# Optimization experiments

Measured on AMD Instinct MI355X. Metric: run time of the kernel, lower is better.

## Reference

```python
import jax, jax.numpy as jnp
import numpy as np

EMBED_DIM = 1024
NUM_HEADS = 16
HEAD_DIM = EMBED_DIM // NUM_HEADS
B, QL, CL = 2, 2048, 2048


def setup_inputs() -> dict:
    key = jax.random.key(0)
    ks = jax.random.split(key, 10)
    s = 1.0 / np.sqrt(EMBED_DIM)  # torch Linear default init scale (approx)
    inp = {
        "query": jax.random.normal(ks[0], (B, QL, EMBED_DIM), jnp.float32),
        "context": jax.random.normal(ks[1], (B, CL, EMBED_DIM), jnp.float32),
        "Wq": jax.random.normal(ks[2], (EMBED_DIM, EMBED_DIM), jnp.float32) * s,
        "bq": jnp.zeros((EMBED_DIM,), jnp.float32),
        "Wk": jax.random.normal(ks[3], (EMBED_DIM, EMBED_DIM), jnp.float32) * s,
        "bk": jnp.zeros((EMBED_DIM,), jnp.float32),
        "Wv": jax.random.normal(ks[4], (EMBED_DIM, EMBED_DIM), jnp.float32) * s,
        "bv": jnp.zeros((EMBED_DIM,), jnp.float32),
        "Wo": jax.random.normal(ks[5], (EMBED_DIM, EMBED_DIM), jnp.float32) * s,
        "bo": jnp.zeros((EMBED_DIM,), jnp.float32),
    }
    return inp


def reference(query, context, Wq, bq, Wk, bk, Wv, bv, Wo, bo):
    b, ql, _ = query.shape
    cl = context.shape[1]
    # projections (torch Linear: x @ W.T + b; here W stored as (in, out) so x @ W + b)
    Q = (query @ Wq + bq).reshape(b, ql, NUM_HEADS, HEAD_DIM).transpose(0, 2, 1, 3)
    K = (context @ Wk + bk).reshape(b, cl, NUM_HEADS, HEAD_DIM).transpose(0, 2, 1, 3)
    V = (context @ Wv + bv).reshape(b, cl, NUM_HEADS, HEAD_DIM).transpose(0, 2, 1, 3)
    # scores [b, h, ql, cl]
    scores = jnp.einsum("bhqd,bhkd->bhqk", Q, K) / np.sqrt(HEAD_DIM).astype(np.float32)
    probs = jax.nn.softmax(scores, axis=-1)
    # dropout=0.0 (eval): identity
    attended = jnp.einsum("bhqk,bhkd->bhqd", probs, V)
    attended = attended.transpose(0, 2, 1, 3).reshape(b, ql, EMBED_DIM)
    return attended @ Wo + bo
```

## Files before the change

### kernel.cpp

```cpp
#include <hip/hip_runtime.h>
#include <hip/hip_bf16.h>
#include <stdint.h>

#define EMBED 1024
#define NH 16
#define HD 64
#define BATCH 2
#define QLEN 2048
#define CLEN 2048

typedef short short8 __attribute__((ext_vector_type(8)));
typedef unsigned short ushort8v __attribute__((ext_vector_type(8)));
typedef float f32x4 __attribute__((ext_vector_type(4)));

__device__ __forceinline__ void async_load16(const void* g, void* l) {
    __builtin_amdgcn_global_load_lds((const __attribute__((address_space(1))) void*)g,
                                     (__attribute__((address_space(3))) void*)l, 16, 0, 0);
}

__global__ void cvt_two(const float* __restrict__ a, __hip_bfloat16* __restrict__ oa,
                        const float* __restrict__ b2, __hip_bfloat16* __restrict__ ob) {
    const float* src = blockIdx.y ? b2 : a;
    __hip_bfloat16* dst = blockIdx.y ? ob : oa;
    int i = (blockIdx.x * 256 + threadIdx.x) * 4;
    float4 v = *(const float4*)(src + i);
    __hip_bfloat16 h[4];
    h[0] = __float2bfloat16(v.x);
    h[1] = __float2bfloat16(v.y);
    h[2] = __float2bfloat16(v.z);
    h[3] = __float2bfloat16(v.w);
    *(ushort4*)(dst + i) = *(const ushort4*)h;
}

__global__ void wtrans4(const float* __restrict__ W0, const float* __restrict__ W1,
                        const float* __restrict__ W2, const float* __restrict__ W3,
                        __hip_bfloat16* __restrict__ T0, __hip_bfloat16* __restrict__ T1,
                        __hip_bfloat16* __restrict__ T2, __hip_bfloat16* __restrict__ T3) {
    const int z = blockIdx.z;
    const float* W = z == 0 ? W0 : z == 1 ? W1 : z == 2 ? W2 : W3;
    __hip_bfloat16* Wt = z == 0 ? T0 : z == 1 ? T1 : z == 2 ? T2 : T3;
    __shared__ float t[32][33];
    const int tx = threadIdx.x, ty = threadIdx.y;
    const int n0 = blockIdx.x * 32, k0 = blockIdx.y * 32;
#pragma unroll
    for (int r = 0; r < 4; r++)
        t[ty * 4 + r][tx] = W[(size_t)(k0 + ty * 4 + r) * EMBED + n0 + tx];
    __syncthreads();
#pragma unroll
    for (int r = 0; r < 4; r++)
        Wt[(size_t)(n0 + ty * 4 + r) * EMBED + k0 + tx] = __float2bfloat16(t[tx][ty * 4 + r]);
}

__global__ __launch_bounds__(256) void vtrans(const __hip_bfloat16* __restrict__ V,
                                              __hip_bfloat16* __restrict__ Vt) {
    __shared__ unsigned short t[64][65];
    const int tid = threadIdx.x;
    const int c0 = blockIdx.x * 64;
    const int b = blockIdx.y >> 4, h = blockIdx.y & 15;
    const int r = tid >> 2;
    const int cs = (tid & 3) * 16;
    const unsigned short* src = (const unsigned short*)V + (size_t)(b * CLEN + c0 + r) * EMBED + h * HD + cs;
    ushort8v v0 = *(const ushort8v*)src;
    ushort8v v1 = *(const ushort8v*)(src + 8);
#pragma unroll
    for (int j = 0; j < 8; j++) { t[r][cs + j] = v0[j]; t[r][cs + 8 + j] = v1[j]; }
    __syncthreads();
    const int d = tid >> 2;
    const int ts = (tid & 3) * 16;
    ushort8v o0, o1;
#pragma unroll
    for (int j = 0; j < 8; j++) { o0[j] = t[ts + j][d]; o1[j] = t[ts + 8 + j][d]; }
    unsigned short* dst = (unsigned short*)Vt + (size_t)((b * NH + h) * HD + d) * CLEN + c0 + ts;
    *(ushort8v*)dst = o0;
    *(ushort8v*)(dst + 8) = o1;
}

__device__ __forceinline__ void store_val(float v, __hip_bfloat16* p) { *p = __float2bfloat16(v); }
__device__ __forceinline__ void store_val(float v, float* p) { *p = v; }

template <typename OutT>
__device__ __forceinline__ void gemm64_body(
    const __hip_bfloat16* __restrict__ A, const __hip_bfloat16* __restrict__ Bt,
    const float* __restrict__ bias, OutT* __restrict__ C,
    int N, int m0, int n0, int cb,
    __hip_bfloat16* As, __hip_bfloat16* Bs) {
    const int K = EMBED;
    const int tid = threadIdx.x;
    const int wave = __builtin_amdgcn_readfirstlane(tid >> 6);
    const int lane = tid & 63, l15 = lane & 15, quad = lane >> 4;
    const int wm = (wave & 1) * 32, wn = (wave >> 1) * 64;
    const int srow = tid >> 2, sseg = (tid & 3) * 8;
    f32x4 acc[2][4] = {};
    for (int k0 = 0; k0 < K; k0 += 32) {
        __syncthreads();
        async_load16(A + (size_t)(m0 + srow) * K + k0 + sseg, As + (size_t)(wave * 64) * 8);
#pragma unroll
        for (int s = 0; s < 2; s++)
            async_load16(Bt + (size_t)(n0 + s * 64 + srow) * K + k0 + sseg,
                         Bs + (size_t)(s * 256 + wave * 64) * 8);
        __syncthreads();
        short8 af[2], bf[4];
#pragma unroll
        for (int t = 0; t < 2; t++)
            af[t] = *(const short8*)(As + (wm + t * 16 + l15) * 32 + quad * 8);
#pragma unroll
        for (int t = 0; t < 4; t++)
            bf[t] = *(const short8*)(Bs + (wn + t * 16 + l15) * 32 + quad * 8);
#pragma unroll
        for (int mt = 0; mt < 2; mt++)
#pragma unroll
            for (int nt = 0; nt < 4; nt++)
                acc[mt][nt] = __builtin_amdgcn_mfma_f32_16x16x32_bf16(af[mt], bf[nt], acc[mt][nt], 0, 0, 0);
    }
#pragma unroll
    for (int mt = 0; mt < 2; mt++) {
#pragma unroll
        for (int nt = 0; nt < 4; nt++) {
            const int c = cb + wn + nt * 16 + l15;
            const float bvv = bias[c];
            const int r0 = m0 + wm + mt * 16 + quad * 4;
#pragma unroll
            for (int r = 0; r < 4; r++)
                store_val(acc[mt][nt][r] + bvv, C + (size_t)(r0 + r) * N + c);
        }
    }
}

__global__ __launch_bounds__(256, 4) void proj_fused(
    const __hip_bfloat16* __restrict__ qbf, const __hip_bfloat16* __restrict__ cbf,
    const __hip_bfloat16* __restrict__ Wqt, const __hip_bfloat16* __restrict__ Wkvt,
    const float* __restrict__ bq, const float* __restrict__ bk, const float* __restrict__ bv,
    __hip_bfloat16* __restrict__ Qp, __hip_bfloat16* __restrict__ Kp, __hip_bfloat16* __restrict__ Vp) {
    __shared__ __hip_bfloat16 As[64 * 32];
    __shared__ __hip_bfloat16 Bs[128 * 32];
    const int blk = blockIdx.x;
    const __hip_bfloat16 *A, *Bt;
    int m0, n0;
    if (blk < 512) {
        A = qbf; Bt = Wqt; m0 = (blk >> 3) * 64; n0 = (blk & 7) * 128;
    } else {
        const int f = blk - 512;
        A = cbf; Bt = Wkvt; m0 = (f >> 4) * 64; n0 = (f & 15) * 128;
    }
    const float* bias;
    __hip_bfloat16* C;
    int cb;
    if (blk < 512) { bias = bq; C = Qp; cb = n0; }
    else if (n0 < 1024) { bias = bk; C = Kp; cb = n0; }
    else { bias = bv; C = Vp; cb = n0 - 1024; }
    gemm64_body<__hip_bfloat16>(A, Bt, bias, C, 1024, m0, n0, cb, As, Bs);
}

__global__ __launch_bounds__(256, 4) void oproj(
    const __hip_bfloat16* __restrict__ A, const __hip_bfloat16* __restrict__ Bt,
    const float* __restrict__ bias, float* __restrict__ C) {
    __shared__ __hip_bfloat16 As[64 * 32];
    __shared__ __hip_bfloat16 Bs[128 * 32];
    const int m0 = blockIdx.y * 64, n0 = blockIdx.x * 128;
    gemm64_body<float>(A, Bt, bias, C, 1024, m0, n0, n0, As, Bs);
}

__global__ __launch_bounds__(256, 4) void flash_attn(
    const __hip_bfloat16* __restrict__ Q, const __hip_bfloat16* __restrict__ K,
    const __hip_bfloat16* __restrict__ Vt, __hip_bfloat16* __restrict__ O) {
    __shared__ __hip_bfloat16 Qs[64 * 64];
    __shared__ __hip_bfloat16 Ks[64 * 64];
    __shared__ __hip_bfloat16 Vts[64 * 64];
    __shared__ __hip_bfloat16 Ps[4 * 16 * 64];
    const int tid = threadIdx.x;
    const int wave = __builtin_amdgcn_readfirstlane(tid >> 6);
    const int lane = tid & 63, l15 = lane & 15, quad = lane >> 4;
    const int s7 = l15 & 7;
    const int b = blockIdx.y >> 4, h = blockIdx.y & 15;
    const int q0 = blockIdx.x * 64;
    const size_t qbase = (size_t)b * QLEN * EMBED + (size_t)h * HD;
    const size_t kbase = (size_t)b * CLEN * EMBED + (size_t)h * HD;
    const size_t vtbase = (size_t)((b * NH + h) * HD) * CLEN;
    const int srow = tid >> 3;
    const int swc = ((tid & 7) ^ ((tid >> 3) & 7)) * 8;

#pragma unroll
    for (int s = 0; s < 2; s++)
        async_load16(Q + qbase + (size_t)(q0 + s * 32 + srow) * EMBED + swc,
                     Qs + (size_t)(s * 256 + wave * 64) * 8);
    __syncthreads();
    short8 qf[2];
#pragma unroll
    for (int ks = 0; ks < 2; ks++)
        qf[ks] = *(const short8*)(Qs + (wave * 16 + l15) * 64 + ((ks * 4 + quad) ^ s7) * 8);

    f32x4 o[4] = {};
    float lsum = 0.f;
    __hip_bfloat16* myP = Ps + wave * 16 * 64;
    const float CEXP = 0.125f * 1.44269504f;

    for (int c0 = 0; c0 < CLEN; c0 += 64) {
        __syncthreads();
#pragma unroll
        for (int s = 0; s < 2; s++) {
            async_load16(K + kbase + (size_t)(c0 + s * 32 + srow) * EMBED + swc,
                         Ks + (size_t)(s * 256 + wave * 64) * 8);
            async_load16(Vt + vtbase + (size_t)(s * 32 + srow) * CLEN + c0 + swc,
                         Vts + (size_t)(s * 256 + wave * 64) * 8);
        }
        __syncthreads();

        f32x4 sc[4] = {};
#pragma unroll
        for (int mc = 0; mc < 4; mc++) {
#pragma unroll
            for (int ks = 0; ks < 2; ks++) {
                short8 kf = *(const short8*)(Ks + (mc * 16 + l15) * 64 + ((ks * 4 + quad) ^ s7) * 8);
                sc[mc] = __builtin_amdgcn_mfma_f32_16x16x32_bf16(kf, qf[ks], sc[mc], 0, 0, 0);
            }
        }

#pragma unroll
        for (int mc = 0; mc < 4; mc++) {
            __hip_bfloat16 pb[4];
#pragma unroll
            for (int r = 0; r < 4; r++) {
                const float p = __builtin_amdgcn_exp2f(sc[mc][r] * CEXP);
                lsum += p;
                pb[r] = __float2bfloat16(p);
            }
            *(ushort4*)(myP + l15 * 64 + (((2 * mc + (quad >> 1)) ^ s7) * 8) + (quad & 1) * 4) =
                *(const ushort4*)pb;
        }

#pragma unroll
        for (int ks = 0; ks < 2; ks++) {
            short8 pf = *(const short8*)(myP + l15 * 64 + ((ks * 4 + quad) ^ s7) * 8);
#pragma unroll
            for (int dm = 0; dm < 4; dm++) {
                short8 vf = *(const short8*)(Vts + (dm * 16 + l15) * 64 + ((ks * 4 + quad) ^ s7) * 8);
                o[dm] = __builtin_amdgcn_mfma_f32_16x16x32_bf16(vf, pf, o[dm], 0, 0, 0);
            }
        }
    }

    lsum += __shfl_xor(lsum, 16);
    lsum += __shfl_xor(lsum, 32);
    const float inv = 1.0f / lsum;
    const int q = q0 + wave * 16 + l15;
    __hip_bfloat16* orow = O + (size_t)(b * QLEN + q) * EMBED + h * HD;
#pragma unroll
    for (int dm = 0; dm < 4; dm++) {
        __hip_bfloat16 ob[4];
#pragma unroll
        for (int r = 0; r < 4; r++) ob[r] = __float2bfloat16(o[dm][r] * inv);
        *(ushort4*)(orow + dm * 16 + quad * 4) = *(const ushort4*)ob;
    }
}

extern "C" void kernel_launch(void* const* d_in, const int* in_sizes, int n_in,
                              void* d_out, int out_size, void* d_ws, size_t ws_size,
                              hipStream_t stream) {
    const float* query = (const float*)d_in[0];
    const float* context = (const float*)d_in[1];
    const float* Wq = (const float*)d_in[2];
    const float* bq = (const float*)d_in[3];
    const float* Wk = (const float*)d_in[4];
    const float* bk = (const float*)d_in[5];
    const float* Wv = (const float*)d_in[6];
    const float* bv = (const float*)d_in[7];
    const float* Wo = (const float*)d_in[8];
    const float* bo = (const float*)d_in[9];
    float* out = (float*)d_out;

    const int NTOK = BATCH * QLEN;
    const int NACT = NTOK * EMBED;
    const int NW = EMBED * EMBED;

    __hip_bfloat16* qbf = (__hip_bfloat16*)d_ws;
    __hip_bfloat16* cbf = qbf + NACT;
    __hip_bfloat16* Wqt = cbf + NACT;
    __hip_bfloat16* Wkt = Wqt + NW;
    __hip_bfloat16* Wvt = Wkt + NW;
    __hip_bfloat16* Wot = Wvt + NW;
    __hip_bfloat16* Qp = Wot + NW;
    __hip_bfloat16* Kp = Qp + NACT;
    __hip_bfloat16* Vtr = Kp + NACT;
    __hip_bfloat16* att = Vtr + NACT;

    cvt_two<<<dim3(NACT / 1024, 2), 256, 0, stream>>>(query, qbf, context, cbf);
    wtrans4<<<dim3(32, 32, 4), dim3(32, 8), 0, stream>>>(Wq, Wk, Wv, Wo, Wqt, Wkt, Wvt, Wot);

    proj_fused<<<1536, 256, 0, stream>>>(qbf, cbf, Wqt, Wkt, bq, bk, bv, Qp, Kp, att);

    vtrans<<<dim3(CLEN / 64, BATCH * NH), 256, 0, stream>>>(att, Vtr);

    flash_attn<<<dim3(QLEN / 64, BATCH * NH), 256, 0, stream>>>(Qp, Kp, Vtr, att);

    oproj<<<dim3(EMBED / 128, NTOK / 64), 256, 0, stream>>>(att, Wot, bo, out);
}
```

Before: 225.9 us.

## Use 32x32 MFMA flash attention with register P and 128x128 projection tiles

```diff
diff --git a/kernel.cpp b/kernel.cpp
--- a/kernel.cpp
+++ b/kernel.cpp
@@ -12,10 +12,20 @@
 typedef short short8 __attribute__((ext_vector_type(8)));
 typedef unsigned short ushort8v __attribute__((ext_vector_type(8)));
 typedef float f32x4 __attribute__((ext_vector_type(4)));
+typedef float f32x16 __attribute__((ext_vector_type(16)));
+typedef uint32_t u32x4 __attribute__((ext_vector_type(4)));
 
 __device__ __forceinline__ void async_load16(const void* g, void* l) {
     __builtin_amdgcn_global_load_lds((const __attribute__((address_space(1))) void*)g,
                                      (__attribute__((address_space(3))) void*)l, 16, 0, 0);
+}
+
+__device__ __forceinline__ uint32_t pack2(float a, float b) {
+    float2 f{a, b};
+    __hip_bfloat162 t = __float22bfloat162_rn(f);
+    uint32_t u;
+    __builtin_memcpy(&u, &t, 4);
+    return u;
 }
 
 __global__ void cvt_two(const float* __restrict__ a, __hip_bfloat16* __restrict__ oa,
@@ -79,7 +89,7 @@
 __device__ __forceinline__ void store_val(float v, float* p) { *p = v; }
 
 template <typename OutT>
-__device__ __forceinline__ void gemm64_body(
+__device__ __forceinline__ void gemm128_body(
     const __hip_bfloat16* __restrict__ A, const __hip_bfloat16* __restrict__ Bt,
     const float* __restrict__ bias, OutT* __restrict__ C,
     int N, int m0, int n0, int cb,
@@ -88,32 +98,33 @@
     const int tid = threadIdx.x;
     const int wave = __builtin_amdgcn_readfirstlane(tid >> 6);
     const int lane = tid & 63, l15 = lane & 15, quad = lane >> 4;
-    const int wm = (wave & 1) * 32, wn = (wave >> 1) * 64;
+    const int wm = (wave >> 1) * 64, wn = (wave & 1) * 64;
     const int srow = tid >> 2, sseg = (tid & 3) * 8;
-    f32x4 acc[2][4] = {};
+    f32x4 acc[4][4] = {};
     for (int k0 = 0; k0 < K; k0 += 32) {
         __syncthreads();
-        async_load16(A + (size_t)(m0 + srow) * K + k0 + sseg, As + (size_t)(wave * 64) * 8);
-#pragma unroll
-        for (int s = 0; s < 2; s++)
+#pragma unroll
+        for (int s = 0; s < 2; s++) {
+            async_load16(A + (size_t)(m0 + s * 64 + srow) * K + k0 + sseg,
+                         As + (size_t)(s * 256 + wave * 64) * 8);
             async_load16(Bt + (size_t)(n0 + s * 64 + srow) * K + k0 + sseg,
                          Bs + (size_t)(s * 256 + wave * 64) * 8);
-        __syncthreads();
-        short8 af[2], bf[4];
-#pragma unroll
-        for (int t = 0; t < 2; t++)
+        }
+        __syncthreads();
+        short8 af[4], bf[4];
+#pragma unroll
+        for (int t = 0; t < 4; t++) {
             af[t] = *(const short8*)(As + (wm + t * 16 + l15) * 32 + quad * 8);
-#pragma unroll
-        for (int t = 0; t < 4; t++)
             bf[t] = *(const short8*)(Bs + (wn + t * 16 + l15) * 32 + quad * 8);
-#pragma unroll
-        for (int mt = 0; mt < 2; mt++)
+        }
+#pragma unroll
+        for (int mt = 0; mt < 4; mt++)
 #pragma unroll
             for (int nt = 0; nt < 4; nt++)
                 acc[mt][nt] = __builtin_amdgcn_mfma_f32_16x16x32_bf16(af[mt], bf[nt], acc[mt][nt], 0, 0, 0);
     }
 #pragma unroll
-    for (int mt = 0; mt < 2; mt++) {
+    for (int mt = 0; mt < 4; mt++) {
 #pragma unroll
         for (int nt = 0; nt < 4; nt++) {
             const int c = cb + wn + nt * 16 + l15;
@@ -126,29 +137,29 @@
     }
 }
 
-__global__ __launch_bounds__(256, 4) void proj_fused(
+__global__ __launch_bounds__(256, 3) void proj128(
     const __hip_bfloat16* __restrict__ qbf, const __hip_bfloat16* __restrict__ cbf,
     const __hip_bfloat16* __restrict__ Wqt, const __hip_bfloat16* __restrict__ Wkvt,
     const float* __restrict__ bq, const float* __restrict__ bk, const float* __restrict__ bv,
     __hip_bfloat16* __restrict__ Qp, __hip_bfloat16* __restrict__ Kp, __hip_bfloat16* __restrict__ Vp) {
-    __shared__ __hip_bfloat16 As[64 * 32];
+    __shared__ __hip_bfloat16 As[128 * 32];
     __shared__ __hip_bfloat16 Bs[128 * 32];
     const int blk = blockIdx.x;
     const __hip_bfloat16 *A, *Bt;
     int m0, n0;
-    if (blk < 512) {
-        A = qbf; Bt = Wqt; m0 = (blk >> 3) * 64; n0 = (blk & 7) * 128;
+    if (blk < 256) {
+        A = qbf; Bt = Wqt; m0 = (blk >> 3) * 128; n0 = (blk & 7) * 128;
     } else {
-        const int f = blk - 512;
-        A = cbf; Bt = Wkvt; m0 = (f >> 4) * 64; n0 = (f & 15) * 128;
+        const int f = blk - 256;
+        A = cbf; Bt = Wkvt; m0 = (f >> 4) * 128; n0 = (f & 15) * 128;
     }
     const float* bias;
     __hip_bfloat16* C;
     int cb;
-    if (blk < 512) { bias = bq; C = Qp; cb = n0; }
+    if (blk < 256) { bias = bq; C = Qp; cb = n0; }
     else if (n0 < 1024) { bias = bk; C = Kp; cb = n0; }
     else { bias = bv; C = Vp; cb = n0 - 1024; }
-    gemm64_body<__hip_bfloat16>(A, Bt, bias, C, 1024, m0, n0, cb, As, Bs);
+    gemm128_body<__hip_bfloat16>(A, Bt, bias, C, 1024, m0, n0, cb, As, Bs);
 }
 
 __global__ __launch_bounds__(256, 4) void oproj(
@@ -156,100 +167,144 @@
     const float* __restrict__ bias, float* __restrict__ C) {
     __shared__ __hip_bfloat16 As[64 * 32];
     __shared__ __hip_bfloat16 Bs[128 * 32];
+    const int K = EMBED, N = EMBED;
     const int m0 = blockIdx.y * 64, n0 = blockIdx.x * 128;
-    gemm64_body<float>(A, Bt, bias, C, 1024, m0, n0, n0, As, Bs);
-}
-
-__global__ __launch_bounds__(256, 4) void flash_attn(
-    const __hip_bfloat16* __restrict__ Q, const __hip_bfloat16* __restrict__ K,
-    const __hip_bfloat16* __restrict__ Vt, __hip_bfloat16* __restrict__ O) {
-    __shared__ __hip_bfloat16 Qs[64 * 64];
-    __shared__ __hip_bfloat16 Ks[64 * 64];
-    __shared__ __hip_bfloat16 Vts[64 * 64];
-    __shared__ __hip_bfloat16 Ps[4 * 16 * 64];
     const int tid = threadIdx.x;
     const int wave = __builtin_amdgcn_readfirstlane(tid >> 6);
     const int lane = tid & 63, l15 = lane & 15, quad = lane >> 4;
-    const int s7 = l15 & 7;
+    const int wm = (wave & 1) * 32, wn = (wave >> 1) * 64;
+    const int srow = tid >> 2, sseg = (tid & 3) * 8;
+    f32x4 acc[2][4] = {};
+    for (int k0 = 0; k0 < K; k0 += 32) {
+        __syncthreads();
+        async_load16(A + (size_t)(m0 + srow) * K + k0 + sseg, As + (size_t)(wave * 64) * 8);
+#pragma unroll
+        for (int s = 0; s < 2; s++)
+            async_load16(Bt + (size_t)(n0 + s * 64 + srow) * K + k0 + sseg,
+                         Bs + (size_t)(s * 256 + wave * 64) * 8);
+        __syncthreads();
+        short8 af[2], bf[4];
+#pragma unroll
+        for (int t = 0; t < 2; t++)
+            af[t] = *(const short8*)(As + (wm + t * 16 + l15) * 32 + quad * 8);
+#pragma unroll
+        for (int t = 0; t < 4; t++)
+            bf[t] = *(const short8*)(Bs + (wn + t * 16 + l15) * 32 + quad * 8);
+#pragma unroll
+        for (int mt = 0; mt < 2; mt++)
+#pragma unroll
+            for (int nt = 0; nt < 4; nt++)
+                acc[mt][nt] = __builtin_amdgcn_mfma_f32_16x16x32_bf16(af[mt], bf[nt], acc[mt][nt], 0, 0, 0);
+    }
+#pragma unroll
+    for (int mt = 0; mt < 2; mt++) {
+#pragma unroll
+        for (int nt = 0; nt < 4; nt++) {
+            const int c = n0 + wn + nt * 16 + l15;
+            const float bvv = bias[c];
+            const int r0 = m0 + wm + mt * 16 + quad * 4;
+#pragma unroll
+            for (int r = 0; r < 4; r++)
+                C[(size_t)(r0 + r) * N + c] = acc[mt][nt][r] + bvv;
+        }
+    }
+}
+
+__global__ __launch_bounds__(128, 2) void flash_attn(
+    const __hip_bfloat16* __restrict__ Q, const __hip_bfloat16* __restrict__ K,
+    const __hip_bfloat16* __restrict__ Vt, __hip_bfloat16* __restrict__ O) {
+    __shared__ __hip_bfloat16 Ks[64 * 64];
+    __shared__ __hip_bfloat16 Vs[64 * 64];
+    const int tid = threadIdx.x;
+    const int wq = __builtin_amdgcn_readfirstlane(tid >> 6);
+    const int lane = tid & 63;
+    const int l31 = lane & 31;
+    const int hbit = lane >> 5;
     const int b = blockIdx.y >> 4, h = blockIdx.y & 15;
     const int q0 = blockIdx.x * 64;
-    const size_t qbase = (size_t)b * QLEN * EMBED + (size_t)h * HD;
     const size_t kbase = (size_t)b * CLEN * EMBED + (size_t)h * HD;
     const size_t vtbase = (size_t)((b * NH + h) * HD) * CLEN;
     const int srow = tid >> 3;
-    const int swc = ((tid & 7) ^ ((tid >> 3) & 7)) * 8;
-
-#pragma unroll
-    for (int s = 0; s < 2; s++)
-        async_load16(Q + qbase + (size_t)(q0 + s * 32 + srow) * EMBED + swc,
-                     Qs + (size_t)(s * 256 + wave * 64) * 8);
-    __syncthreads();
-    short8 qf[2];
-#pragma unroll
-    for (int ks = 0; ks < 2; ks++)
-        qf[ks] = *(const short8*)(Qs + (wave * 16 + l15) * 64 + ((ks * 4 + quad) ^ s7) * 8);
-
-    f32x4 o[4] = {};
+    const int sg = (tid & 7) ^ (srow & 7);
+    const int ldsoff = (tid & 64) * 8;
+
+    const __hip_bfloat16* qptr =
+        Q + (size_t)(b * QLEN + q0 + wq * 32 + l31) * EMBED + h * HD + hbit * 8;
+    short8 qf[4];
+#pragma unroll
+    for (int t = 0; t < 4; t++) qf[t] = *(const short8*)(qptr + t * 16);
+
+    f32x16 o[2] = {};
     float lsum = 0.f;
-    __hip_bfloat16* myP = Ps + wave * 16 * 64;
     const float CEXP = 0.125f * 1.44269504f;
 
     for (int c0 = 0; c0 < CLEN; c0 += 64) {
         __syncthreads();
 #pragma unroll
-        for (int s = 0; s < 2; s++) {
-            async_load16(K + kbase + (size_t)(c0 + s * 32 + srow) * EMBED + swc,
-                         Ks + (size_t)(s * 256 + wave * 64) * 8);
-            async_load16(Vt + vtbase + (size_t)(s * 32 + srow) * CLEN + c0 + swc,
-                         Vts + (size_t)(s * 256 + wave * 64) * 8);
-        }
-        __syncthreads();
-
-        f32x4 sc[4] = {};
-#pragma unroll
-        for (int mc = 0; mc < 4; mc++) {
-#pragma unroll
-            for (int ks = 0; ks < 2; ks++) {
-                short8 kf = *(const short8*)(Ks + (mc * 16 + l15) * 64 + ((ks * 4 + quad) ^ s7) * 8);
-                sc[mc] = __builtin_amdgcn_mfma_f32_16x16x32_bf16(kf, qf[ks], sc[mc], 0, 0, 0);
+        for (int i = 0; i < 4; i++) {
+            async_load16(K + kbase + (size_t)(c0 + i * 16 + srow) * EMBED + sg * 8,
+                         Ks + i * 1024 + ldsoff);
+            async_load16(Vt + vtbase + (size_t)(i * 16 + srow) * CLEN + c0 + sg * 8,
+                         Vs + i * 1024 + ldsoff);
+        }
+        __syncthreads();
+
+#pragma unroll
+        for (int mc = 0; mc < 2; mc++) {
+            const int row = mc * 32 + l31;
+            const __hip_bfloat16* kr = Ks + row * 64;
+            f32x16 s = {};
+#pragma unroll
+            for (int kc = 0; kc < 4; kc++) {
+                short8 kf = *(const short8*)(kr + ((2 * kc + hbit) ^ (row & 7)) * 8);
+                s = __builtin_amdgcn_mfma_f32_32x32x16_bf16(kf, qf[kc], s, 0, 0, 0);
             }
-        }
-
-#pragma unroll
-        for (int mc = 0; mc < 4; mc++) {
-            __hip_bfloat16 pb[4];
-#pragma unroll
-            for (int r = 0; r < 4; r++) {
-                const float p = __builtin_amdgcn_exp2f(sc[mc][r] * CEXP);
-                lsum += p;
-                pb[r] = __float2bfloat16(p);
+            uint32_t dw[8];
+#pragma unroll
+            for (int i = 0; i < 8; i++) {
+                const float p0 = __builtin_amdgcn_exp2f(s[2 * i] * CEXP);
+                const float p1 = __builtin_amdgcn_exp2f(s[2 * i + 1] * CEXP);
+                lsum += p0 + p1;
+                dw[i] = pack2(p0, p1);
             }
-            *(ushort4*)(myP + l15 * 64 + (((2 * mc + (quad >> 1)) ^ s7) * 8) + (quad & 1) * 4) =
-                *(const ushort4*)pb;
-        }
-
-#pragma unroll
-        for (int ks = 0; ks < 2; ks++) {
-            short8 pf = *(const short8*)(myP + l15 * 64 + ((ks * 4 + quad) ^ s7) * 8);
-#pragma unroll
-            for (int dm = 0; dm < 4; dm++) {
-                short8 vf = *(const short8*)(Vts + (dm * 16 + l15) * 64 + ((ks * 4 + quad) ^ s7) * 8);
-                o[dm] = __builtin_amdgcn_mfma_f32_16x16x32_bf16(vf, pf, o[dm], 0, 0, 0);
+#pragma unroll
+            for (int tp = 0; tp < 2; tp++) {
+                const uint32_t a0 = hbit ? dw[4 * tp + 2] : dw[4 * tp + 0];
+                const uint32_t a1 = hbit ? dw[4 * tp + 3] : dw[4 * tp + 1];
+                const uint32_t b0 = hbit ? dw[4 * tp + 0] : dw[4 * tp + 2];
+                const uint32_t b1 = hbit ? dw[4 * tp + 1] : dw[4 * tp + 3];
+                const uint32_t x0 = (uint32_t)__shfl_xor((int)b0, 32);
+                const uint32_t x1 = (uint32_t)__shfl_xor((int)b1, 32);
+                u32x4 fb;
+                fb[0] = hbit ? x0 : a0;
+                fb[1] = hbit ? x1 : a1;
+                fb[2] = hbit ? a0 : x0;
+                fb[3] = hbit ? a1 : x1;
+                const short8 pfr = __builtin_bit_cast(short8, fb);
+                const int kc = mc * 2 + tp;
+#pragma unroll
+                for (int dm = 0; dm < 2; dm++) {
+                    const int vrow = dm * 32 + l31;
+                    short8 vf = *(const short8*)(Vs + vrow * 64 + ((2 * kc + hbit) ^ (vrow & 7)) * 8);
+                    o[dm] = __builtin_amdgcn_mfma_f32_32x32x16_bf16(vf, pfr, o[dm], 0, 0, 0);
+                }
             }
         }
     }
 
-    lsum += __shfl_xor(lsum, 16);
     lsum += __shfl_xor(lsum, 32);
     const float inv = 1.0f / lsum;
-    const int q = q0 + wave * 16 + l15;
+    const int q = q0 + wq * 32 + l31;
     __hip_bfloat16* orow = O + (size_t)(b * QLEN + q) * EMBED + h * HD;
 #pragma unroll
-    for (int dm = 0; dm < 4; dm++) {
-        __hip_bfloat16 ob[4];
-#pragma unroll
-        for (int r = 0; r < 4; r++) ob[r] = __float2bfloat16(o[dm][r] * inv);
-        *(ushort4*)(orow + dm * 16 + quad * 4) = *(const ushort4*)ob;
+    for (int dm = 0; dm < 2; dm++) {
+#pragma unroll
+        for (int g = 0; g < 4; g++) {
+            __hip_bfloat16 ob[4];
+#pragma unroll
+            for (int r = 0; r < 4; r++) ob[r] = __float2bfloat16(o[dm][g * 4 + r] * inv);
+            *(ushort4*)(orow + dm * 32 + hbit * 4 + g * 8) = *(const ushort4*)ob;
+        }
     }
 }
 
@@ -286,11 +341,11 @@
     cvt_two<<<dim3(NACT / 1024, 2), 256, 0, stream>>>(query, qbf, context, cbf);
     wtrans4<<<dim3(32, 32, 4), dim3(32, 8), 0, stream>>>(Wq, Wk, Wv, Wo, Wqt, Wkt, Wvt, Wot);
 
-    proj_fused<<<1536, 256, 0, stream>>>(qbf, cbf, Wqt, Wkt, bq, bk, bv, Qp, Kp, att);
+    proj128<<<768, 256, 0, stream>>>(qbf, cbf, Wqt, Wkt, bq, bk, bv, Qp, Kp, att);
 
     vtrans<<<dim3(CLEN / 64, BATCH * NH), 256, 0, stream>>>(att, Vtr);
 
-    flash_attn<<<dim3(QLEN / 64, BATCH * NH), 256, 0, stream>>>(Qp, Kp, Vtr, att);
+    flash_attn<<<dim3(QLEN / 64, BATCH * NH), 128, 0, stream>>>(Qp, Kp, Vtr, att);
 
     oproj<<<dim3(EMBED / 128, NTOK / 64), 256, 0, stream>>>(att, Wot, bo, out);
 }
```

New measurement: 227.8 us. No clear change (+0.8%).
